# Kernel tuning notes

Hardware: AMD Instinct MI355X
Metric: run time of the kernel (lower is better)

The kernel has to match this reference:

```python
import jax, jax.numpy as jnp
import numpy as np

COEF_MEMORY = 0.2

def setup_inputs() -> dict:
    key = jax.random.key(0)
    k1, k2, k3, k4 = jax.random.split(key, 4)
    B, T, HW, C, Cv, M = 2, 8, 4096, 64, 3, 1024
    k = jax.random.normal(k1, (B, T, HW, C), dtype=jnp.float32)
    v = jax.random.normal(k2, (B, T, HW, Cv), dtype=jnp.float32)
    m_k = jax.random.normal(k3, (B, T - 1, M, C), dtype=jnp.float32)
    m_v = jax.random.normal(k4, (B, T - 1, M, Cv), dtype=jnp.float32)
    return {"k": k, "v": v, "m_k": m_k, "m_v": m_v}

def reference(k, v, m_k, m_v):
    # k: [B,T,HW,C] frame keys; v: [B,T,HW,Cv] frame values (quarter-res images)
    # m_k: [B,T-1,M,C] memory keys at step i; m_v: [B,T-1,M,Cv] memory values
    c = COEF_MEMORY
    k_i = k[:, :-1]  # ref keys  [B,T-1,HW,C]
    k_j = k[:, 1:]   # tar keys  [B,T-1,HW,C]
    v_i = v[:, :-1]  # ref vals  [B,T-1,HW,Cv]
    # frame-to-frame affinity: softmax over ref positions (last axis)
    sim_k = jax.nn.softmax(jnp.einsum('btqc,btkc->btqk', k_j, k_i), axis=-1)
    # memory-to-frame affinity: softmax over memory slots
    sim_m = jax.nn.softmax(jnp.einsum('btqc,btmc->btqm', k_j, m_k), axis=-1)
    rec_k = jnp.einsum('btqk,btkd->btqd', sim_k, v_i)   # [B,T-1,HW,Cv]
    rec_m = jnp.einsum('btqm,btmd->btqd', sim_m, m_v)   # [B,T-1,HW,Cv]
    return (1.0 - c) * rec_k + c * rec_m
```

## Files before the change

### kernel.cpp

```cpp
#include <hip/hip_runtime.h>

typedef __attribute__((ext_vector_type(2))) __fp16 h2;
typedef __attribute__((ext_vector_type(4))) __fp16 h4;
typedef __attribute__((ext_vector_type(8))) __fp16 h8;
typedef __attribute__((ext_vector_type(4))) float f32x4;

#define LOG2E 1.44269504088896340736f

#define WS_K    0ull
#define WS_MK   7340032ull
#define WS_VT   9175040ull
#define WS_MVT  9633792ull
#define WS_NEED 9748480ull

__device__ __forceinline__ h2 pkrtz(float a, float b) {
    return __builtin_bit_cast(h2, __builtin_amdgcn_cvt_pkrtz(a, b));
}

__device__ __forceinline__ void gll16(const void* g, void* l) {
    __builtin_amdgcn_global_load_lds(
        (const __attribute__((address_space(1))) unsigned int*)g,
        (__attribute__((address_space(3))) unsigned int*)l, 16, 0, 0);
}

__global__ __launch_bounds__(256) void kast_pre_kernel(
    const float* __restrict__ K, const float* __restrict__ V,
    const float* __restrict__ MK, const float* __restrict__ MV,
    char* __restrict__ ws)
{
    const int id = blockIdx.x * 256 + threadIdx.x;
    if (id < 573440) {
        const bool ismk = id >= 458752;
        const int lid = ismk ? id - 458752 : id;
        const int c = lid & 7;
        const int r = (lid >> 3) & 63;
        int kt, s;
        if (ismk) { kt = (lid >> 9) & 15; s = lid >> 13; }
        else      { kt = (lid >> 9) & 63; s = lid >> 15; }
        const int b = s / 7, t = s - b * 7;
        const float* src = ismk
            ? MK + (((size_t)(b * 7 + t) * 1024 + kt * 64 + r) * 64 + c * 8)
            : K  + (((size_t)(b * 8 + t) * 4096 + kt * 64 + r) * 64 + c * 8);
        const f32x4 xa = *(const f32x4*)src;
        const f32x4 xb = *(const f32x4*)(src + 4);
        const h2 q0 = pkrtz(xa[0], xa[1]), q1 = pkrtz(xa[2], xa[3]);
        const h2 q2 = pkrtz(xb[0], xb[1]), q3 = pkrtz(xb[2], xb[3]);
        const h8 out = {q0[0], q0[1], q1[0], q1[1], q2[0], q2[1], q3[0], q3[1]};
        __fp16* dst = (__fp16*)(ws + (ismk ? WS_MK : WS_K))
                    + (size_t)(ismk ? (s * 16 + kt) : (s * 64 + kt)) * 4096
                    + r * 64 + ((c ^ (r & 7)) * 8);
        *(h8*)dst = out;
    } else {
        const int vid = id - 573440;
        const bool ismv = vid >= 57344;
        const int lid = ismv ? vid - 57344 : vid;
        const int c = lid & 15;
        const int d = (lid >> 4) & 3;
        int kt, s;
        if (ismv) { kt = (lid >> 6) & 15; s = lid >> 10; }
        else      { kt = (lid >> 6) & 63; s = lid >> 12; }
        const int b = s / 7, t = s - b * 7;
        const float* src = ismv
            ? MV + (((size_t)(b * 7 + t) * 1024 + kt * 64 + c * 4) * 3)
            : V  + (((size_t)(b * 8 + t) * 4096 + kt * 64 + c * 4) * 3);
        float f0, f1, f2, f3;
        if (d == 3) { f0 = f1 = f2 = f3 = 1.0f; }
        else { f0 = src[d]; f1 = src[3 + d]; f2 = src[6 + d]; f3 = src[9 + d]; }
        const h2 pa = pkrtz(f0, f1), pb = pkrtz(f2, f3);
        const h4 out4 = {pa[0], pa[1], pb[0], pb[1]};
        __fp16* dst = (__fp16*)(ws + (ismv ? WS_MVT : WS_VT))
                    + (size_t)(ismv ? (s * 16 + kt) : (s * 64 + kt)) * 256
                    + d * 64 + (4 * ((c >> 2) ^ d) + (c & 3)) * 4;
        *(h4*)dst = out4;
    }
}

__global__ __launch_bounds__(256) void kast_attn_kernel(
    const float* __restrict__ K,
    const char* __restrict__ ws,
    float* __restrict__ OUT)
{
    __shared__ alignas(16) __fp16 sK2[2][64][64];
    __shared__ alignas(16) __fp16 sVT2[2][4][64];

    const int id = blockIdx.x;
    const int sw = (id & 7) * 112 + (id >> 3);
    const int bt = sw >> 6;
    const int qblk = sw & 63;
    const int b = bt / 7, t = bt - b * 7;

    const int tid = threadIdx.x;
    const int lane = tid & 63;
    const int w = tid >> 6;
    const int col = lane & 15;
    const int g = lane >> 4;
    const int cs = col & 7;
    const int d3 = col & 3;

    const float* qp = K + (((size_t)b * 8 + (t + 1)) * 4096 + (size_t)(qblk * 64 + w * 16 + col)) * 64;
    h8 aq[2];
#pragma unroll
    for (int ch = 0; ch < 2; ++ch) {
        const int cc = ch * 32 + g * 8;
        const f32x4 xa = *(const f32x4*)&qp[cc];
        const f32x4 xb = *(const f32x4*)&qp[cc + 4];
        const h2 p0 = pkrtz(xa[0] * LOG2E, xa[1] * LOG2E);
        const h2 p1 = pkrtz(xa[2] * LOG2E, xa[3] * LOG2E);
        const h2 p2 = pkrtz(xb[0] * LOG2E, xb[1] * LOG2E);
        const h2 p3 = pkrtz(xb[2] * LOG2E, xb[3] * LOG2E);
        aq[ch] = (h8){p0[0], p0[1], p1[0], p1[1], p2[0], p2[1], p3[0], p3[1]};
    }

    float outc0 = 0.f, outc1 = 0.f, outc2 = 0.f;

    auto stageK = [&](const char* kb, int tkt, int buf) {
        const char* ksrc = kb + (size_t)tkt * 8192 + w * 2048 + lane * 16;
        char* kdst = ((char*)&sK2[buf][0][0]) + w * 2048 + lane * 16;
        gll16(ksrc, kdst);
        gll16(ksrc + 1024, kdst + 1024);
    };

    for (int phase = 0; phase < 2; ++phase) {
        const char* kbase; const char* vbase; int ntile; float wgt;
        if (phase == 0) {
            kbase = ws + WS_K  + (size_t)bt * 64 * 8192;
            vbase = ws + WS_VT + (size_t)bt * 64 * 512;
            ntile = 64; wgt = 0.8f;
        } else {
            kbase = ws + WS_MK  + (size_t)bt * 16 * 8192;
            vbase = ws + WS_MVT + (size_t)bt * 16 * 512;
            ntile = 16; wgt = 0.2f;
        }

        stageK(kbase, 0, 0);
        if (tid < 32)
            ((f32x4*)&sVT2[0][0][0])[tid] = ((const f32x4*)vbase)[tid];
        __syncthreads();

        float mrun = -1e30f;
        f32x4 O = (f32x4){0.f, 0.f, 0.f, 0.f};

        for (int kt = 0; kt < ntile; ++kt) {
            const int cur = kt & 1;
            const int nb = cur ^ 1;

            if (kt + 1 < ntile) {
                stageK(kbase, kt + 1, nb);
                if (tid < 32)
                    ((f32x4*)&sVT2[nb][0][0])[tid] =
                        ((const f32x4*)(vbase + (size_t)(kt + 1) * 512))[tid];
            }

            f32x4 acc[4];
#pragma unroll
            for (int nt = 0; nt < 4; ++nt) acc[nt] = (f32x4){0.f, 0.f, 0.f, 0.f};
            __builtin_amdgcn_s_setprio(1);
#pragma unroll
            for (int ch = 0; ch < 2; ++ch) {
                h8 bh[4];
#pragma unroll
                for (int nt = 0; nt < 4; ++nt)
                    bh[nt] = *(const h8*)&sK2[cur][nt * 16 + col][((ch * 4 + g) ^ cs) * 8];
#pragma unroll
                for (int nt = 0; nt < 4; ++nt)
                    acc[nt] = __builtin_amdgcn_mfma_f32_16x16x32_f16(bh[nt], aq[ch], acc[nt], 0, 0, 0);
            }
            __builtin_amdgcn_s_setprio(0);

            {
                float tm = acc[0][0];
#pragma unroll
                for (int nt = 0; nt < 4; ++nt)
#pragma unroll
                    for (int j = 0; j < 4; ++j) tm = fmaxf(tm, acc[nt][j]);
                tm = fmaxf(tm, __shfl_xor(tm, 16));
                tm = fmaxf(tm, __shfl_xor(tm, 32));
                if (!__all(tm <= mrun)) {
                    const float mnew = fmaxf(mrun, tm);
                    const float sc = __builtin_amdgcn_exp2f(mrun - mnew);
                    O *= sc;
                    mrun = mnew;
                }
            }

            const char* vtb = (const char*)&sVT2[cur][0][0] + d3 * 128;
#pragma unroll
            for (int nt = 0; nt < 4; ++nt) {
                const float p0 = __builtin_amdgcn_exp2f(acc[nt][0] - mrun);
                const float p1 = __builtin_amdgcn_exp2f(acc[nt][1] - mrun);
                const float p2 = __builtin_amdgcn_exp2f(acc[nt][2] - mrun);
                const float p3 = __builtin_amdgcn_exp2f(acc[nt][3] - mrun);
                const h2 pa = pkrtz(p0, p1), pb = pkrtz(p2, p3);
                const h4 pf = (h4){pa[0], pa[1], pb[0], pb[1]};
                const h4 vf = *(const h4*)(vtb + (4 * (nt ^ d3) + g) * 8);
                O = __builtin_amdgcn_mfma_f32_16x16x16f16(vf, pf, O, 0, 0, 0);
            }

            __syncthreads();
        }

        const float inv = wgt / O[3];
        outc0 += O[0] * inv;
        outc1 += O[1] * inv;
        outc2 += O[2] * inv;
    }

    if (g == 0) {
        const int q = qblk * 64 + w * 16 + col;
        float* op = OUT + (((size_t)b * 7 + t) * 4096 + (size_t)q) * 3;
        op[0] = outc0; op[1] = outc1; op[2] = outc2;
    }
}

__global__ __launch_bounds__(256) void kast_attn_fb(
    const float* __restrict__ K, const float* __restrict__ V,
    const float* __restrict__ MK, const float* __restrict__ MV,
    float* __restrict__ OUT)
{
    __shared__ alignas(16) __fp16 sK[2][64][64];
    __shared__ alignas(16) __fp16 sVT[2][4][68];

    const int id = blockIdx.x;
    const int sw = (id & 7) * 112 + (id >> 3);
    const int bt = sw >> 6;
    const int qblk = sw & 63;
    const int b = bt / 7, t = bt % 7;

    const int tid = threadIdx.x;
    const int lane = tid & 63;
    const int w = tid >> 6;
    const int col = lane & 15;
    const int g = lane >> 4;

    const int r = tid >> 2;
    const int c0 = (tid & 3) * 16;
    const int rs = (r & 7) << 3;
    const unsigned vr = (unsigned)tid / 3u;
    const unsigned vd = (unsigned)tid - vr * 3u;

    if (tid < 128) sVT[tid >> 6][3][tid & 63] = (__fp16)1.0f;

    const float* Qbase = K + (((size_t)b * 8 + (t + 1)) * 4096) * 64;
    h8 aq[2];
    {
        const int qrow = qblk * 64 + w * 16 + col;
        const float* qp = Qbase + (size_t)qrow * 64;
#pragma unroll
        for (int ch = 0; ch < 2; ++ch) {
            const int cc = ch * 32 + g * 8;
            const f32x4 xa = *(const f32x4*)&qp[cc];
            const f32x4 xb = *(const f32x4*)&qp[cc + 4];
            const h2 p0 = pkrtz(xa[0] * LOG2E, xa[1] * LOG2E);
            const h2 p1 = pkrtz(xa[2] * LOG2E, xa[3] * LOG2E);
            const h2 p2 = pkrtz(xb[0] * LOG2E, xb[1] * LOG2E);
            const h2 p3 = pkrtz(xb[2] * LOG2E, xb[3] * LOG2E);
            aq[ch] = (h8){p0[0], p0[1], p1[0], p1[1], p2[0], p2[1], p3[0], p3[1]};
        }
    }

    float outc0 = 0.f, outc1 = 0.f, outc2 = 0.f;

    for (int phase = 0; phase < 2; ++phase) {
        const float* kp; const float* vp; int ntile; float wgt;
        if (phase == 0) {
            kp = K + (((size_t)b * 8 + t) * 4096) * 64;
            vp = V + (((size_t)b * 8 + t) * 4096) * 3;
            ntile = 64; wgt = 0.8f;
        } else {
            kp = MK + (((size_t)b * 7 + t) * 1024) * 64;
            vp = MV + (((size_t)b * 7 + t) * 1024) * 3;
            ntile = 16; wgt = 0.2f;
        }
        {
            const float* src = kp + ((size_t)r) * 64 + c0;
            const f32x4* s4 = (const f32x4*)src;
            const f32x4 ra = s4[0], rb = s4[1], rc = s4[2], rd = s4[3];
            const h2 q0 = pkrtz(ra[0], ra[1]), q1 = pkrtz(ra[2], ra[3]);
            const h2 q2 = pkrtz(rb[0], rb[1]), q3 = pkrtz(rb[2], rb[3]);
            const h2 q4 = pkrtz(rc[0], rc[1]), q5 = pkrtz(rc[2], rc[3]);
            const h2 q6 = pkrtz(rd[0], rd[1]), q7 = pkrtz(rd[2], rd[3]);
            *(h8*)&sK[0][r][c0 ^ rs] = (h8){q0[0], q0[1], q1[0], q1[1], q2[0], q2[1], q3[0], q3[1]};
            *(h8*)&sK[0][r][(c0 + 8) ^ rs] = (h8){q4[0], q4[1], q5[0], q5[1], q6[0], q6[1], q7[0], q7[1]};
            if (tid < 192) sVT[0][vd][vr] = (__fp16)vp[tid];
        }
        __syncthreads();

        float mrun = -1e30f;
        f32x4 O = (f32x4){0.f, 0.f, 0.f, 0.f};

        for (int kt = 0; kt < ntile; ++kt) {
            const int cur = kt & 1;
            const bool have = (kt + 1) < ntile;
            f32x4 ra, rb, rc, rd; float rv = 0.f;
            if (have) {
                const float* src = kp + ((size_t)(kt + 1) * 64 + r) * 64 + c0;
                const f32x4* s4 = (const f32x4*)src;
                ra = s4[0]; rb = s4[1]; rc = s4[2]; rd = s4[3];
                if (tid < 192) rv = vp[(size_t)(kt + 1) * 192 + tid];
            }
            f32x4 acc[4];
#pragma unroll
            for (int nt = 0; nt < 4; ++nt) acc[nt] = (f32x4){0.f, 0.f, 0.f, 0.f};
#pragma unroll
            for (int ch = 0; ch < 2; ++ch) {
                h8 bh[4];
#pragma unroll
                for (int nt = 0; nt < 4; ++nt) {
                    const int rr = nt * 16 + col;
                    const int cc = (ch * 32 + g * 8) ^ ((rr & 7) << 3);
                    bh[nt] = *(const h8*)&sK[cur][rr][cc];
                }
#pragma unroll
                for (int nt = 0; nt < 4; ++nt)
                    acc[nt] = __builtin_amdgcn_mfma_f32_16x16x32_f16(bh[nt], aq[ch], acc[nt], 0, 0, 0);
            }
            {
                float tm = acc[0][0];
#pragma unroll
                for (int nt = 0; nt < 4; ++nt)
#pragma unroll
                    for (int j = 0; j < 4; ++j) tm = fmaxf(tm, acc[nt][j]);
                tm = fmaxf(tm, __shfl_xor(tm, 16));
                tm = fmaxf(tm, __shfl_xor(tm, 32));
                if (!__all(tm <= mrun)) {
                    const float mnew = fmaxf(mrun, tm);
                    const float sc = __builtin_amdgcn_exp2f(mrun - mnew);
                    O *= sc;
                    mrun = mnew;
                }
            }
#pragma unroll
            for (int nt = 0; nt < 4; ++nt) {
                const float p0 = __builtin_amdgcn_exp2f(acc[nt][0] - mrun);
                const float p1 = __builtin_amdgcn_exp2f(acc[nt][1] - mrun);
                const float p2 = __builtin_amdgcn_exp2f(acc[nt][2] - mrun);
                const float p3 = __builtin_amdgcn_exp2f(acc[nt][3] - mrun);
                const h2 pa = pkrtz(p0, p1), pb = pkrtz(p2, p3);
                const h4 pf = (h4){pa[0], pa[1], pb[0], pb[1]};
                const h4 vf = *(const h4*)&sVT[cur][col & 3][nt * 16 + 4 * g];
                O = __builtin_amdgcn_mfma_f32_16x16x16f16(vf, pf, O, 0, 0, 0);
            }
            if (have) {
                const int nb = cur ^ 1;
                const h2 q0 = pkrtz(ra[0], ra[1]), q1 = pkrtz(ra[2], ra[3]);
                const h2 q2 = pkrtz(rb[0], rb[1]), q3 = pkrtz(rb[2], rb[3]);
                const h2 q4 = pkrtz(rc[0], rc[1]), q5 = pkrtz(rc[2], rc[3]);
                const h2 q6 = pkrtz(rd[0], rd[1]), q7 = pkrtz(rd[2], rd[3]);
                *(h8*)&sK[nb][r][c0 ^ rs] = (h8){q0[0], q0[1], q1[0], q1[1], q2[0], q2[1], q3[0], q3[1]};
                *(h8*)&sK[nb][r][(c0 + 8) ^ rs] = (h8){q4[0], q4[1], q5[0], q5[1], q6[0], q6[1], q7[0], q7[1]};
                if (tid < 192) sVT[nb][vd][vr] = (__fp16)rv;
            }
            __syncthreads();
        }
        const float inv = wgt / O[3];
        outc0 += O[0] * inv;
        outc1 += O[1] * inv;
        outc2 += O[2] * inv;
    }

    if (g == 0) {
        const int q = qblk * 64 + w * 16 + col;
        float* op = OUT + (((size_t)b * 7 + t) * 4096 + (size_t)q) * 3;
        op[0] = outc0; op[1] = outc1; op[2] = outc2;
    }
}

extern "C" void kernel_launch(void* const* d_in, const int* in_sizes, int n_in,
                              void* d_out, int out_size, void* d_ws, size_t ws_size,
                              hipStream_t stream) {
    const float* K  = (const float*)d_in[0];
    const float* V  = (const float*)d_in[1];
    const float* MK = (const float*)d_in[2];
    const float* MV = (const float*)d_in[3];
    float* OUT = (float*)d_out;
    if (ws_size >= WS_NEED) {
        hipLaunchKernelGGL(kast_pre_kernel, dim3(2520), dim3(256), 0, stream,
                           K, V, MK, MV, (char*)d_ws);
        hipLaunchKernelGGL(kast_attn_kernel, dim3(896), dim3(256), 0, stream,
                           K, (const char*)d_ws, OUT);
    } else {
        hipLaunchKernelGGL(kast_attn_fb, dim3(896), dim3(256), 0, stream,
                           K, V, MK, MV, OUT);
    }
}
```

Baseline: 119.0 us.

## Split key tiles across two wave groups per block with LDS softmax merge

The attention block grows from 256 to 512 threads. Two groups of four waves each process half of the key tiles and half of the memory slots for the same 64 queries, and their running max and partial sums are combined through LDS at the end (flash-decoding style). This halves each wave's serial tile loop and doubles the waves in flight per block, addressing latency on a grid of only 896 blocks. The costs are twice the LDS per block, a final merge step, and loading the same query registers twice.

```diff
diff --git a/kernel.cpp b/kernel.cpp
--- a/kernel.cpp
+++ b/kernel.cpp
@@ -75,13 +75,14 @@
     }
 }
 
-__global__ __launch_bounds__(256) void kast_attn_kernel(
+__global__ __launch_bounds__(512) void kast_attn_kernel(
     const float* __restrict__ K,
     const char* __restrict__ ws,
     float* __restrict__ OUT)
 {
-    __shared__ alignas(16) __fp16 sK2[2][64][64];
-    __shared__ alignas(16) __fp16 sVT2[2][4][64];
+    __shared__ alignas(16) __fp16 sK2[2][2][64][64];
+    __shared__ alignas(16) __fp16 sVT2[2][2][4][64];
+    __shared__ float mrg[8][16][10];
 
     const int id = blockIdx.x;
     const int sw = (id & 7) * 112 + (id >> 3);
@@ -92,12 +93,14 @@
     const int tid = threadIdx.x;
     const int lane = tid & 63;
     const int w = tid >> 6;
+    const int h = w >> 2;
+    const int wl = w & 3;
     const int col = lane & 15;
     const int g = lane >> 4;
     const int cs = col & 7;
     const int d3 = col & 3;
 
-    const float* qp = K + (((size_t)b * 8 + (t + 1)) * 4096 + (size_t)(qblk * 64 + w * 16 + col)) * 64;
+    const float* qp = K + (((size_t)b * 8 + (t + 1)) * 4096 + (size_t)(qblk * 64 + wl * 16 + col)) * 64;
     h8 aq[2];
 #pragma unroll
     for (int ch = 0; ch < 2; ++ch) {
@@ -111,30 +114,30 @@
         aq[ch] = (h8){p0[0], p0[1], p1[0], p1[1], p2[0], p2[1], p3[0], p3[1]};
     }
 
-    float outc0 = 0.f, outc1 = 0.f, outc2 = 0.f;
-
-    auto stageK = [&](const char* kb, int tkt, int buf) {
-        const char* ksrc = kb + (size_t)tkt * 8192 + w * 2048 + lane * 16;
-        char* kdst = ((char*)&sK2[buf][0][0]) + w * 2048 + lane * 16;
+    auto stage = [&](const char* kb, const char* vb, int tkt, int buf) {
+        const char* ksrc = kb + (size_t)tkt * 8192 + wl * 2048 + lane * 16;
+        char* kdst = ((char*)&sK2[h][buf][0][0]) + wl * 2048 + lane * 16;
         gll16(ksrc, kdst);
         gll16(ksrc + 1024, kdst + 1024);
+        if (wl == 0 && lane < 32)
+            ((f32x4*)&sVT2[h][buf][0][0])[lane] =
+                ((const f32x4*)(vb + (size_t)tkt * 512))[lane];
     };
 
+#pragma unroll
     for (int phase = 0; phase < 2; ++phase) {
-        const char* kbase; const char* vbase; int ntile; float wgt;
+        const char* kbase; const char* vbase; int ntile;
         if (phase == 0) {
-            kbase = ws + WS_K  + (size_t)bt * 64 * 8192;
-            vbase = ws + WS_VT + (size_t)bt * 64 * 512;
-            ntile = 64; wgt = 0.8f;
+            ntile = 32;
+            kbase = ws + WS_K  + ((size_t)bt * 64 + h * 32) * 8192;
+            vbase = ws + WS_VT + ((size_t)bt * 64 + h * 32) * 512;
         } else {
-            kbase = ws + WS_MK  + (size_t)bt * 16 * 8192;
-            vbase = ws + WS_MVT + (size_t)bt * 16 * 512;
-            ntile = 16; wgt = 0.2f;
-        }
-
-        stageK(kbase, 0, 0);
-        if (tid < 32)
-            ((f32x4*)&sVT2[0][0][0])[tid] = ((const f32x4*)vbase)[tid];
+            ntile = 8;
+            kbase = ws + WS_MK  + ((size_t)bt * 16 + h * 8) * 8192;
+            vbase = ws + WS_MVT + ((size_t)bt * 16 + h * 8) * 512;
+        }
+
+        stage(kbase, vbase, 0, 0);
         __syncthreads();
 
         float mrun = -1e30f;
@@ -144,12 +147,7 @@
             const int cur = kt & 1;
             const int nb = cur ^ 1;
 
-            if (kt + 1 < ntile) {
-                stageK(kbase, kt + 1, nb);
-                if (tid < 32)
-                    ((f32x4*)&sVT2[nb][0][0])[tid] =
-                        ((const f32x4*)(vbase + (size_t)(kt + 1) * 512))[tid];
-            }
+            if (kt + 1 < ntile) stage(kbase, vbase, kt + 1, nb);
 
             f32x4 acc[4];
 #pragma unroll
@@ -160,7 +158,7 @@
                 h8 bh[4];
 #pragma unroll
                 for (int nt = 0; nt < 4; ++nt)
-                    bh[nt] = *(const h8*)&sK2[cur][nt * 16 + col][((ch * 4 + g) ^ cs) * 8];
+                    bh[nt] = *(const h8*)&sK2[h][cur][nt * 16 + col][((ch * 4 + g) ^ cs) * 8];
 #pragma unroll
                 for (int nt = 0; nt < 4; ++nt)
                     acc[nt] = __builtin_amdgcn_mfma_f32_16x16x32_f16(bh[nt], aq[ch], acc[nt], 0, 0, 0);
@@ -183,7 +181,7 @@
                 }
             }
 
-            const char* vtb = (const char*)&sVT2[cur][0][0] + d3 * 128;
+            const char* vtb = (const char*)&sVT2[h][cur][0][0] + d3 * 128;
 #pragma unroll
             for (int nt = 0; nt < 4; ++nt) {
                 const float p0 = __builtin_amdgcn_exp2f(acc[nt][0] - mrun);
@@ -199,16 +197,33 @@
             __syncthreads();
         }
 
-        const float inv = wgt / O[3];
-        outc0 += O[0] * inv;
-        outc1 += O[1] * inv;
-        outc2 += O[2] * inv;
-    }
-
-    if (g == 0) {
+        if (g == 0) {
+            float* m5 = &mrg[w][col][phase * 5];
+            m5[0] = mrun; m5[1] = O[0]; m5[2] = O[1]; m5[3] = O[2]; m5[4] = O[3];
+        }
+    }
+
+    __syncthreads();
+    if (w < 4 && g == 0) {
+        const float* A = &mrg[w][col][0];
+        const float* B = &mrg[w + 4][col][0];
+        float o0 = 0.f, o1 = 0.f, o2 = 0.f;
+#pragma unroll
+        for (int p = 0; p < 2; ++p) {
+            const float wgt = p ? 0.2f : 0.8f;
+            const float ma = A[p * 5], mb = B[p * 5];
+            const float m = fmaxf(ma, mb);
+            const float ea = __builtin_amdgcn_exp2f(ma - m);
+            const float eb = __builtin_amdgcn_exp2f(mb - m);
+            const float l = A[p * 5 + 4] * ea + B[p * 5 + 4] * eb;
+            const float inv = wgt / l;
+            o0 += (A[p * 5 + 1] * ea + B[p * 5 + 1] * eb) * inv;
+            o1 += (A[p * 5 + 2] * ea + B[p * 5 + 2] * eb) * inv;
+            o2 += (A[p * 5 + 3] * ea + B[p * 5 + 3] * eb) * inv;
+        }
         const int q = qblk * 64 + w * 16 + col;
         float* op = OUT + (((size_t)b * 7 + t) * 4096 + (size_t)q) * 3;
-        op[0] = outc0; op[1] = outc1; op[2] = outc2;
+        op[0] = o0; op[1] = o1; op[2] = o2;
     }
 }
 
@@ -376,7 +391,7 @@
     if (ws_size >= WS_NEED) {
         hipLaunchKernelGGL(kast_pre_kernel, dim3(2520), dim3(256), 0, stream,
                            K, V, MK, MV, (char*)d_ws);
-        hipLaunchKernelGGL(kast_attn_kernel, dim3(896), dim3(256), 0, stream,
+        hipLaunchKernelGGL(kast_attn_kernel, dim3(896), dim3(512), 0, stream,
                            K, (const char*)d_ws, OUT);
     } else {
         hipLaunchKernelGGL(kast_attn_fb, dim3(896), dim3(256), 0, stream,
```

After: 96.87 us. -18.6%, faster.

## Split keys across waves with register loads and merge softmax partials in LDS

Applied to the files above, without the earlier changes.

The attention kernel is restructured so each block handles 32 queries, and each of the four waves processes a quarter of the key range for all of them. Key and value fragments come straight from global memory into registers with a two-stage software prefetch, so the shared-memory staging and the per-tile __syncthreads are gone. Partial max, sum and output for each wave are merged through a small LDS buffer using a log-sum-exp combine. The grid doubles to 1792 blocks and launch bounds request 4 blocks per CU. The cost is extra register pressure, direct global loads that rely on the cache for reuse, and the conditional skip of the max rescale is replaced by an unconditional rescale.

```diff
diff --git a/kernel.cpp b/kernel.cpp
--- a/kernel.cpp
+++ b/kernel.cpp
@@ -15,12 +15,6 @@
 
 __device__ __forceinline__ h2 pkrtz(float a, float b) {
     return __builtin_bit_cast(h2, __builtin_amdgcn_cvt_pkrtz(a, b));
-}
-
-__device__ __forceinline__ void gll16(const void* g, void* l) {
-    __builtin_amdgcn_global_load_lds(
-        (const __attribute__((address_space(1))) unsigned int*)g,
-        (__attribute__((address_space(3))) unsigned int*)l, 16, 0, 0);
 }
 
 __global__ __launch_bounds__(256) void kast_pre_kernel(
@@ -75,18 +69,17 @@
     }
 }
 
-__global__ __launch_bounds__(256) void kast_attn_kernel(
+__global__ __launch_bounds__(256, 4) void kast_attn_kernel(
     const float* __restrict__ K,
     const char* __restrict__ ws,
     float* __restrict__ OUT)
 {
-    __shared__ alignas(16) __fp16 sK2[2][64][64];
-    __shared__ alignas(16) __fp16 sVT2[2][4][64];
+    __shared__ float mrg[4][32][5];
 
     const int id = blockIdx.x;
-    const int sw = (id & 7) * 112 + (id >> 3);
-    const int bt = sw >> 6;
-    const int qblk = sw & 63;
+    const int sw = (id & 7) * 224 + (id >> 3);
+    const int bt = sw >> 7;
+    const int qblk = sw & 127;
     const int b = bt / 7, t = bt - b * 7;
 
     const int tid = threadIdx.x;
@@ -97,118 +90,187 @@
     const int cs = col & 7;
     const int d3 = col & 3;
 
-    const float* qp = K + (((size_t)b * 8 + (t + 1)) * 4096 + (size_t)(qblk * 64 + w * 16 + col)) * 64;
-    h8 aq[2];
-#pragma unroll
-    for (int ch = 0; ch < 2; ++ch) {
-        const int cc = ch * 32 + g * 8;
-        const f32x4 xa = *(const f32x4*)&qp[cc];
-        const f32x4 xb = *(const f32x4*)&qp[cc + 4];
-        const h2 p0 = pkrtz(xa[0] * LOG2E, xa[1] * LOG2E);
-        const h2 p1 = pkrtz(xa[2] * LOG2E, xa[3] * LOG2E);
-        const h2 p2 = pkrtz(xb[0] * LOG2E, xb[1] * LOG2E);
-        const h2 p3 = pkrtz(xb[2] * LOG2E, xb[3] * LOG2E);
-        aq[ch] = (h8){p0[0], p0[1], p1[0], p1[1], p2[0], p2[1], p3[0], p3[1]};
-    }
-
-    float outc0 = 0.f, outc1 = 0.f, outc2 = 0.f;
-
-    auto stageK = [&](const char* kb, int tkt, int buf) {
-        const char* ksrc = kb + (size_t)tkt * 8192 + w * 2048 + lane * 16;
-        char* kdst = ((char*)&sK2[buf][0][0]) + w * 2048 + lane * 16;
-        gll16(ksrc, kdst);
-        gll16(ksrc + 1024, kdst + 1024);
-    };
-
+    const int a00 = col * 128 + ((g ^ cs) * 16);
+    const int a10 = col * 128 + (((4 + g) ^ cs) * 16);
+    const int ov0 = (4 * (0 ^ d3) + g) * 8;
+    const int ov1 = (4 * (1 ^ d3) + g) * 8;
+    const int ov2 = (4 * (2 ^ d3) + g) * 8;
+    const int ov3 = (4 * (3 ^ d3) + g) * 8;
+
+    h8 aq00, aq01, aq10, aq11;
+    {
+        const float* qp0 = K + (((size_t)b * 8 + (t + 1)) * 4096
+                          + (size_t)(qblk * 32 + col)) * 64;
+        const float* qp1 = qp0 + 16 * 64;
+#pragma unroll
+        for (int mt = 0; mt < 2; ++mt) {
+            const float* qp = mt ? qp1 : qp0;
+#pragma unroll
+            for (int ch = 0; ch < 2; ++ch) {
+                const int cc = ch * 32 + g * 8;
+                const f32x4 xa = *(const f32x4*)&qp[cc];
+                const f32x4 xb = *(const f32x4*)&qp[cc + 4];
+                const h2 p0 = pkrtz(xa[0] * LOG2E, xa[1] * LOG2E);
+                const h2 p1 = pkrtz(xa[2] * LOG2E, xa[3] * LOG2E);
+                const h2 p2 = pkrtz(xb[0] * LOG2E, xb[1] * LOG2E);
+                const h2 p3 = pkrtz(xb[2] * LOG2E, xb[3] * LOG2E);
+                const h8 f = {p0[0], p0[1], p1[0], p1[1], p2[0], p2[1], p3[0], p3[1]};
+                if (mt == 0 && ch == 0) aq00 = f;
+                else if (mt == 0)       aq01 = f;
+                else if (ch == 0)       aq10 = f;
+                else                    aq11 = f;
+            }
+        }
+    }
+
+    float oa0 = 0.f, oa1 = 0.f, oa2 = 0.f;
+
+#pragma unroll
     for (int phase = 0; phase < 2; ++phase) {
-        const char* kbase; const char* vbase; int ntile; float wgt;
-        if (phase == 0) {
-            kbase = ws + WS_K  + (size_t)bt * 64 * 8192;
-            vbase = ws + WS_VT + (size_t)bt * 64 * 512;
-            ntile = 64; wgt = 0.8f;
-        } else {
-            kbase = ws + WS_MK  + (size_t)bt * 16 * 8192;
-            vbase = ws + WS_MVT + (size_t)bt * 16 * 512;
-            ntile = 16; wgt = 0.2f;
-        }
-
-        stageK(kbase, 0, 0);
-        if (tid < 32)
-            ((f32x4*)&sVT2[0][0][0])[tid] = ((const f32x4*)vbase)[tid];
+        const int n = phase ? 8 : 32;
+        const float wgt = phase ? 0.2f : 0.8f;
+        const char* kbase = phase
+            ? ws + WS_MK  + (size_t)bt * 131072 + (size_t)w * 32768
+            : ws + WS_K   + (size_t)bt * 524288 + (size_t)w * 131072;
+        const char* vbase = (phase
+            ? ws + WS_MVT + (size_t)bt * 8192  + (size_t)w * 2048
+            : ws + WS_VT  + (size_t)bt * 32768 + (size_t)w * 8192) + d3 * 128;
+
+        float mrun0 = -1e30f, mrun1 = -1e30f;
+        f32x4 O0 = (f32x4){0.f,0.f,0.f,0.f}, O1 = (f32x4){0.f,0.f,0.f,0.f};
+
+        h8 kA00, kA01, kA10, kA11; h4 vA0, vA1;
+        {
+            const char* tb = kbase;
+            kA00 = *(const h8*)(tb + a00);
+            kA01 = *(const h8*)(tb + a00 + 2048);
+            kA10 = *(const h8*)(tb + a10);
+            kA11 = *(const h8*)(tb + a10 + 2048);
+            vA0 = *(const h4*)(vbase + ov0);
+            vA1 = *(const h4*)(vbase + ov1);
+        }
+
+#define COMPUTE(kf00, kf01, kf10, kf11, v0, v1)                                   \
+        {                                                                         \
+            f32x4 c00 = (f32x4){0.f,0.f,0.f,0.f}, c01 = c00, c10 = c00, c11 = c00;\
+            __builtin_amdgcn_s_setprio(1);                                        \
+            c00 = __builtin_amdgcn_mfma_f32_16x16x32_f16(kf00, aq00, c00, 0,0,0); \
+            c01 = __builtin_amdgcn_mfma_f32_16x16x32_f16(kf01, aq00, c01, 0,0,0); \
+            c10 = __builtin_amdgcn_mfma_f32_16x16x32_f16(kf00, aq10, c10, 0,0,0); \
+            c11 = __builtin_amdgcn_mfma_f32_16x16x32_f16(kf01, aq10, c11, 0,0,0); \
+            c00 = __builtin_amdgcn_mfma_f32_16x16x32_f16(kf10, aq01, c00, 0,0,0); \
+            c01 = __builtin_amdgcn_mfma_f32_16x16x32_f16(kf11, aq01, c01, 0,0,0); \
+            c10 = __builtin_amdgcn_mfma_f32_16x16x32_f16(kf10, aq11, c10, 0,0,0); \
+            c11 = __builtin_amdgcn_mfma_f32_16x16x32_f16(kf11, aq11, c11, 0,0,0); \
+            __builtin_amdgcn_s_setprio(0);                                        \
+            float tm0 = fmaxf(fmaxf(fmaxf(c00[0], c00[1]), fmaxf(c00[2], c00[3])),\
+                              fmaxf(fmaxf(c01[0], c01[1]), fmaxf(c01[2], c01[3])));\
+            float tm1 = fmaxf(fmaxf(fmaxf(c10[0], c10[1]), fmaxf(c10[2], c10[3])),\
+                              fmaxf(fmaxf(c11[0], c11[1]), fmaxf(c11[2], c11[3])));\
+            float s0 = __shfl_xor(tm0, 16), s1 = __shfl_xor(tm1, 16);             \
+            tm0 = fmaxf(tm0, s0); tm1 = fmaxf(tm1, s1);                           \
+            s0 = __shfl_xor(tm0, 32); s1 = __shfl_xor(tm1, 32);                   \
+            tm0 = fmaxf(tm0, s0); tm1 = fmaxf(tm1, s1);                           \
+            const float m0 = fmaxf(mrun0, tm0), m1 = fmaxf(mrun1, tm1);           \
+            const float r0 = __builtin_amdgcn_exp2f(mrun0 - m0);                  \
+            const float r1 = __builtin_amdgcn_exp2f(mrun1 - m1);                  \
+            O0 *= r0; O1 *= r1; mrun0 = m0; mrun1 = m1;                           \
+            {                                                                     \
+                const float e0 = __builtin_amdgcn_exp2f(c00[0] - mrun0);          \
+                const float e1 = __builtin_amdgcn_exp2f(c00[1] - mrun0);          \
+                const float e2 = __builtin_amdgcn_exp2f(c00[2] - mrun0);          \
+                const float e3 = __builtin_amdgcn_exp2f(c00[3] - mrun0);          \
+                const h2 pa = pkrtz(e0, e1), pb = pkrtz(e2, e3);                  \
+                const h4 pf = (h4){pa[0], pa[1], pb[0], pb[1]};                   \
+                O0 = __builtin_amdgcn_mfma_f32_16x16x16f16(v0, pf, O0, 0, 0, 0);  \
+            }                                                                     \
+            {                                                                     \
+                const float e0 = __builtin_amdgcn_exp2f(c01[0] - mrun0);          \
+                const float e1 = __builtin_amdgcn_exp2f(c01[1] - mrun0);          \
+                const float e2 = __builtin_amdgcn_exp2f(c01[2] - mrun0);          \
+                const float e3 = __builtin_amdgcn_exp2f(c01[3] - mrun0);          \
+                const h2 pa = pkrtz(e0, e1), pb = pkrtz(e2, e3);                  \
+                const h4 pf = (h4){pa[0], pa[1], pb[0], pb[1]};                   \
+                O0 = __builtin_amdgcn_mfma_f32_16x16x16f16(v1, pf, O0, 0, 0, 0);  \
+            }                                                                     \
+            {                                                                     \
+                const float e0 = __builtin_amdgcn_exp2f(c10[0] - mrun1);          \
+                const float e1 = __builtin_amdgcn_exp2f(c10[1] - mrun1);          \
+                const float e2 = __builtin_amdgcn_exp2f(c10[2] - mrun1);          \
+                const float e3 = __builtin_amdgcn_exp2f(c10[3] - mrun1);          \
+                const h2 pa = pkrtz(e0, e1), pb = pkrtz(e2, e3);                  \
+                const h4 pf = (h4){pa[0], pa[1], pb[0], pb[1]};                   \
+                O1 = __builtin_amdgcn_mfma_f32_16x16x16f16(v0, pf, O1, 0, 0, 0);  \
+            }                                                                     \
+            {                                                                     \
+                const float e0 = __builtin_amdgcn_exp2f(c11[0] - mrun1);          \
+                const float e1 = __builtin_amdgcn_exp2f(c11[1] - mrun1);          \
+                const float e2 = __builtin_amdgcn_exp2f(c11[2] - mrun1);          \
+                const float e3 = __builtin_amdgcn_exp2f(c11[3] - mrun1);          \
+                const h2 pa = pkrtz(e0, e1), pb = pkrtz(e2, e3);                  \
+                const h4 pf = (h4){pa[0], pa[1], pb[0], pb[1]};                   \
+                O1 = __builtin_amdgcn_mfma_f32_16x16x16f16(v1, pf, O1, 0, 0, 0);  \
+            }                                                                     \
+        }
+
+        for (int kt = 0; kt < n; kt += 2) {
+            h8 kB00, kB01, kB10, kB11; h4 vB0, vB1;
+            {
+                const char* tb = kbase + (size_t)(kt + 1) * 4096;
+                kB00 = *(const h8*)(tb + a00);
+                kB01 = *(const h8*)(tb + a00 + 2048);
+                kB10 = *(const h8*)(tb + a10);
+                kB11 = *(const h8*)(tb + a10 + 2048);
+                const char* vt = vbase + (size_t)(kt >> 1) * 512;
+                vB0 = *(const h4*)(vt + ov2);
+                vB1 = *(const h4*)(vt + ov3);
+            }
+            COMPUTE(kA00, kA01, kA10, kA11, vA0, vA1);
+            if (kt + 2 < n) {
+                const char* tb = kbase + (size_t)(kt + 2) * 4096;
+                kA00 = *(const h8*)(tb + a00);
+                kA01 = *(const h8*)(tb + a00 + 2048);
+                kA10 = *(const h8*)(tb + a10);
+                kA11 = *(const h8*)(tb + a10 + 2048);
+                const char* vt = vbase + (size_t)((kt + 2) >> 1) * 512;
+                vA0 = *(const h4*)(vt + ov0);
+                vA1 = *(const h4*)(vt + ov1);
+            }
+            COMPUTE(kB00, kB01, kB10, kB11, vB0, vB1);
+        }
+#undef COMPUTE
+
+        if (g == 0) {
+            float* m5a = &mrg[w][col][0];
+            m5a[0] = mrun0;
+            m5a[1] = O0[0]; m5a[2] = O0[1]; m5a[3] = O0[2]; m5a[4] = O0[3];
+            float* m5b = &mrg[w][16 + col][0];
+            m5b[0] = mrun1;
+            m5b[1] = O1[0]; m5b[2] = O1[1]; m5b[3] = O1[2]; m5b[4] = O1[3];
+        }
         __syncthreads();
-
-        float mrun = -1e30f;
-        f32x4 O = (f32x4){0.f, 0.f, 0.f, 0.f};
-
-        for (int kt = 0; kt < ntile; ++kt) {
-            const int cur = kt & 1;
-            const int nb = cur ^ 1;
-
-            if (kt + 1 < ntile) {
-                stageK(kbase, kt + 1, nb);
-                if (tid < 32)
-                    ((f32x4*)&sVT2[nb][0][0])[tid] =
-                        ((const f32x4*)(vbase + (size_t)(kt + 1) * 512))[tid];
-            }
-
-            f32x4 acc[4];
-#pragma unroll
-            for (int nt = 0; nt < 4; ++nt) acc[nt] = (f32x4){0.f, 0.f, 0.f, 0.f};
-            __builtin_amdgcn_s_setprio(1);
-#pragma unroll
-            for (int ch = 0; ch < 2; ++ch) {
-                h8 bh[4];
-#pragma unroll
-                for (int nt = 0; nt < 4; ++nt)
-                    bh[nt] = *(const h8*)&sK2[cur][nt * 16 + col][((ch * 4 + g) ^ cs) * 8];
-#pragma unroll
-                for (int nt = 0; nt < 4; ++nt)
-                    acc[nt] = __builtin_amdgcn_mfma_f32_16x16x32_f16(bh[nt], aq[ch], acc[nt], 0, 0, 0);
-            }
-            __builtin_amdgcn_s_setprio(0);
-
-            {
-                float tm = acc[0][0];
-#pragma unroll
-                for (int nt = 0; nt < 4; ++nt)
-#pragma unroll
-                    for (int j = 0; j < 4; ++j) tm = fmaxf(tm, acc[nt][j]);
-                tm = fmaxf(tm, __shfl_xor(tm, 16));
-                tm = fmaxf(tm, __shfl_xor(tm, 32));
-                if (!__all(tm <= mrun)) {
-                    const float mnew = fmaxf(mrun, tm);
-                    const float sc = __builtin_amdgcn_exp2f(mrun - mnew);
-                    O *= sc;
-                    mrun = mnew;
-                }
-            }
-
-            const char* vtb = (const char*)&sVT2[cur][0][0] + d3 * 128;
-#pragma unroll
-            for (int nt = 0; nt < 4; ++nt) {
-                const float p0 = __builtin_amdgcn_exp2f(acc[nt][0] - mrun);
-                const float p1 = __builtin_amdgcn_exp2f(acc[nt][1] - mrun);
-                const float p2 = __builtin_amdgcn_exp2f(acc[nt][2] - mrun);
-                const float p3 = __builtin_amdgcn_exp2f(acc[nt][3] - mrun);
-                const h2 pa = pkrtz(p0, p1), pb = pkrtz(p2, p3);
-                const h4 pf = (h4){pa[0], pa[1], pb[0], pb[1]};
-                const h4 vf = *(const h4*)(vtb + (4 * (nt ^ d3) + g) * 8);
-                O = __builtin_amdgcn_mfma_f32_16x16x16f16(vf, pf, O, 0, 0, 0);
-            }
-
-            __syncthreads();
-        }
-
-        const float inv = wgt / O[3];
-        outc0 += O[0] * inv;
-        outc1 += O[1] * inv;
-        outc2 += O[2] * inv;
-    }
-
-    if (g == 0) {
-        const int q = qblk * 64 + w * 16 + col;
+        if (tid < 32) {
+            float m = -1e30f;
+#pragma unroll
+            for (int q4 = 0; q4 < 4; ++q4) m = fmaxf(m, mrg[q4][tid][0]);
+            float l = 0.f, r0 = 0.f, r1 = 0.f, r2 = 0.f;
+#pragma unroll
+            for (int q4 = 0; q4 < 4; ++q4) {
+                const float* m5 = &mrg[q4][tid][0];
+                const float e = __builtin_amdgcn_exp2f(m5[0] - m);
+                r0 += m5[1] * e; r1 += m5[2] * e; r2 += m5[3] * e;
+                l  += m5[4] * e;
+            }
+            const float inv = wgt / l;
+            oa0 += r0 * inv; oa1 += r1 * inv; oa2 += r2 * inv;
+        }
+        __syncthreads();
+    }
+
+    if (tid < 32) {
+        const int q = qblk * 32 + tid;
         float* op = OUT + (((size_t)b * 7 + t) * 4096 + (size_t)q) * 3;
-        op[0] = outc0; op[1] = outc1; op[2] = outc2;
+        op[0] = oa0; op[1] = oa1; op[2] = oa2;
     }
 }
 
@@ -376,7 +438,7 @@
     if (ws_size >= WS_NEED) {
         hipLaunchKernelGGL(kast_pre_kernel, dim3(2520), dim3(256), 0, stream,
                            K, V, MK, MV, (char*)d_ws);
-        hipLaunchKernelGGL(kast_attn_kernel, dim3(896), dim3(256), 0, stream,
+        hipLaunchKernelGGL(kast_attn_kernel, dim3(1792), dim3(256), 0, stream,
                            K, (const char*)d_ws, OUT);
     } else {
         hipLaunchKernelGGL(kast_attn_fb, dim3(896), dim3(256), 0, stream,
```

New measurement: 98.29 us. 1.21x faster.
